# Performance work log

Hardware: AMD Instinct MI355X
Metric: run time of the kernel (lower is better)

The kernel has to match this reference:

```python
import jax, jax.numpy as jnp
import numpy as np

DIM = 1024
HEADS = 16
DIM_HEAD = 64
INNER = HEADS * DIM_HEAD  # 1024
EPS = 1e-5


def setup_inputs() -> dict:
    key = jax.random.key(0)
    ks = jax.random.split(key, 5)
    x = jax.random.normal(ks[0], (4, 2048, DIM), dtype=jnp.float32)
    ln_gamma = jnp.ones((DIM,), dtype=jnp.float32)
    ln_beta = jnp.zeros((DIM,), dtype=jnp.float32)
    # nn.Linear weights ~ U(-1/sqrt(fan_in), 1/sqrt(fan_in)); stored as (out, in) in torch,
    # here kept as (in, out) for x @ W.
    lim = 1.0 / np.sqrt(DIM)
    w_qkv = jax.random.uniform(ks[1], (DIM, 3 * INNER), minval=-lim, maxval=lim, dtype=jnp.float32)
    lim2 = 1.0 / np.sqrt(INNER)
    w_out = jax.random.uniform(ks[2], (INNER, DIM), minval=-lim2, maxval=lim2, dtype=jnp.float32)
    return {"x": x, "ln_gamma": ln_gamma, "ln_beta": ln_beta, "w_qkv": w_qkv, "w_out": w_out}


def reference(x, ln_gamma, ln_beta, w_qkv, w_out):
    b, n, d = x.shape
    # LayerNorm
    mu = jnp.mean(x, axis=-1, keepdims=True)
    var = jnp.mean(jnp.square(x - mu), axis=-1, keepdims=True)
    xn = (x - mu) * jax.lax.rsqrt(var + EPS) * ln_gamma + ln_beta
    # QKV projection
    qkv = xn @ w_qkv  # (b, n, 3*inner)
    q, k, v = jnp.split(qkv, 3, axis=-1)
    def to_heads(t):
        return t.reshape(b, n, HEADS, DIM_HEAD).transpose(0, 2, 1, 3)  # (b,h,n,dh)
    q, k, v = to_heads(q), to_heads(k), to_heads(v)
    scale = DIM_HEAD ** -0.5
    scores = jnp.einsum('bhqd,bhkd->bhqk', q, k) * scale
    causal = jnp.tril(jnp.ones((n, n), dtype=bool))
    scores = jnp.where(causal, scores, -jnp.inf)
    probs = jax.nn.softmax(scores, axis=-1)
    out = jnp.einsum('bhqk,bhkd->bhqd', probs, v)
    out = out.transpose(0, 2, 1, 3).reshape(b, n, INNER)
    return out @ w_out
```

## Files before the change

### kernel.cpp

```cpp
#include <hip/hip_runtime.h>
#include <hip/hip_bf16.h>

#define DIM 1024
#define HEADS 16
#define DH 64
#define SEQ 2048
#define BATCH 4
#define ROWS (BATCH * SEQ)
#define NQKV (3 * DIM)

typedef __attribute__((ext_vector_type(8))) __bf16 bf16x8;
typedef __attribute__((ext_vector_type(4))) __bf16 bf16x4;
typedef __attribute__((ext_vector_type(4))) float f32x4;

__device__ inline void gload16(const void* g, void* l) {
  __builtin_amdgcn_global_load_lds(
      (const __attribute__((address_space(1))) void*)g,
      (__attribute__((address_space(3))) void*)l, 16, 0, 0);
}

__device__ inline float fast_exp2(float x) {
#if __has_builtin(__builtin_amdgcn_exp2f)
  return __builtin_amdgcn_exp2f(x);
#else
  return exp2f(x);
#endif
}

__global__ __launch_bounds__(256) void ln_tc(
    const float* __restrict__ x, const float* __restrict__ gamma,
    const float* __restrict__ beta, __bf16* __restrict__ xnb,
    const float* __restrict__ wq, const float* __restrict__ wo,
    __bf16* __restrict__ qT, __bf16* __restrict__ oT) {
  __shared__ float red1[4], red2[4];
  __shared__ float tile[32][33];
  const int bid = blockIdx.x;
  const int tid = threadIdx.x;
  if (bid < ROWS) {
    const float4* xr = (const float4*)(x + (size_t)bid * DIM);
    float4 v = xr[tid];
    float s1 = v.x + v.y + v.z + v.w;
    float s2 = v.x * v.x + v.y * v.y + v.z * v.z + v.w * v.w;
#pragma unroll
    for (int d = 32; d > 0; d >>= 1) {
      s1 += __shfl_xor(s1, d);
      s2 += __shfl_xor(s2, d);
    }
    const int wave = tid >> 6, lane = tid & 63;
    if (lane == 0) { red1[wave] = s1; red2[wave] = s2; }
    __syncthreads();
    s1 = red1[0] + red1[1] + red1[2] + red1[3];
    s2 = red2[0] + red2[1] + red2[2] + red2[3];
    const float mean = s1 * (1.0f / DIM);
    const float var = s2 * (1.0f / DIM) - mean * mean;
    const float rstd = rsqrtf(var + 1e-5f);
    float4 g = ((const float4*)gamma)[tid];
    float4 b = ((const float4*)beta)[tid];
    bf16x4 o;
    o[0] = (__bf16)((v.x - mean) * rstd * g.x + b.x);
    o[1] = (__bf16)((v.y - mean) * rstd * g.y + b.y);
    o[2] = (__bf16)((v.z - mean) * rstd * g.z + b.z);
    o[3] = (__bf16)((v.w - mean) * rstd * g.w + b.w);
    *(bf16x4*)(xnb + (size_t)bid * DIM + tid * 4) = o;
  } else {
    const int id2 = bid - ROWS;
    int bx = id2 & 127;
    const int by = id2 >> 7;
    const int tx = tid & 31, ty = tid >> 5;
    const float* in;
    __bf16* out;
    int cols;
    if (bx < 96) {
      in = wq; out = qT; cols = NQKV;
    } else {
      in = wo; out = oT; cols = DIM; bx -= 96;
    }
    const int c0 = bx * 32, r0 = by * 32;
#pragma unroll
    for (int rr = ty; rr < 32; rr += 8)
      tile[rr][tx] = in[(size_t)(r0 + rr) * cols + c0 + tx];
    __syncthreads();
#pragma unroll
    for (int rr = ty; rr < 32; rr += 8)
      out[(size_t)(c0 + rr) * DIM + r0 + tx] = (__bf16)tile[tx][rr];
  }
}

template <int MODE>
__global__ __launch_bounds__(512, 1) void gemmP(
    const __bf16* __restrict__ A, const __bf16* __restrict__ Bt, const int K,
    const int N, float* __restrict__ Cout, __bf16* __restrict__ qb,
    __bf16* __restrict__ kb, __bf16* __restrict__ vtb) {
  __shared__ __bf16 As[3][2][128 * 64];
  __shared__ __bf16 Bs[3][128 * 64];
  const int tid = threadIdx.x;
  const int wave = tid >> 6, lane = tid & 63;
  const int quad = lane >> 4, l16 = lane & 15;
  const int wm = wave >> 2, wn = wave & 3;

  const int i = (int)blockIdx.x;
  const int xcd = i & 7;
  const int j = i >> 3;
  const int ntn = N >> 7;
  const int mgrp = j / ntn;
  const int ntl = j - mgrp * ntn;
  const size_t tileM = (size_t)(xcd + (mgrp << 3)) * 256;
  const size_t tileN = (size_t)ntl * 128;
  const int sel = (MODE == 1) ? (int)(tileN >> 10) : 0;
  const bool vmode = (MODE == 1) && (sel == 2);

  f32x4 acc[8][2];
#pragma unroll
  for (int a = 0; a < 8; ++a)
#pragma unroll
    for (int b = 0; b < 2; ++b) acc[a][b] = (f32x4){0.f, 0.f, 0.f, 0.f};

  const __bf16* Abase = A + tileM * (size_t)K;
  const __bf16* Bbase = Bt + tileN * (size_t)K;

  const int slr = tid >> 3, sc = tid & 7;
  const int scol = (sc ^ (slr & 7)) << 3;

  auto stageA = [&](int buf, int h, int kt) {
    const size_t col = (size_t)(kt << 6) + scol;
#pragma unroll
    for (int p = 0; p < 2; ++p) {
      const int gr = p * 128 + h * 64 + slr;
      const int lr = p * 64 + slr;
      gload16(Abase + (size_t)gr * K + col, &As[buf][h][lr * 64 + sc * 8]);
    }
  };
  auto stageB = [&](int buf, int kt) {
    const size_t col = (size_t)(kt << 6) + scol;
#pragma unroll
    for (int p = 0; p < 2; ++p) {
      const int lr = p * 64 + slr;
      gload16(Bbase + (size_t)lr * K + col, &Bs[buf][lr * 64 + sc * 8]);
    }
  };
  auto stageTile = [&](int buf, int kt) {
    stageA(buf, 0, kt);
    stageB(buf, kt);
    stageA(buf, 1, kt);
  };

  const int rpc = quad ^ (l16 & 7);
  auto ldA = [&](int buf, int mt, int ks) -> bf16x8 {
    const int lr = wm * 64 + (mt & 3) * 16 + l16;
    return *(const bf16x8*)&As[buf][mt >> 2][lr * 64 + ((rpc ^ (ks << 2)) << 3)];
  };
  auto ldB = [&](int buf, int nt, int ks) -> bf16x8 {
    const int lr = wn * 32 + nt * 16 + l16;
    return *(const bf16x8*)&Bs[buf][lr * 64 + ((rpc ^ (ks << 2)) << 3)];
  };

  auto cluster = [&](const bf16x8* af, bf16x8 bf0, bf16x8 bf1, int mb) {
    __builtin_amdgcn_s_setprio(1);
    if (vmode) {
#pragma unroll
      for (int mt = 0; mt < 4; ++mt) {
        acc[mb + mt][0] = __builtin_amdgcn_mfma_f32_16x16x32_bf16(
            af[mt], bf0, acc[mb + mt][0], 0, 0, 0);
        acc[mb + mt][1] = __builtin_amdgcn_mfma_f32_16x16x32_bf16(
            af[mt], bf1, acc[mb + mt][1], 0, 0, 0);
      }
    } else {
#pragma unroll
      for (int mt = 0; mt < 4; ++mt) {
        acc[mb + mt][0] = __builtin_amdgcn_mfma_f32_16x16x32_bf16(
            bf0, af[mt], acc[mb + mt][0], 0, 0, 0);
        acc[mb + mt][1] = __builtin_amdgcn_mfma_f32_16x16x32_bf16(
            bf1, af[mt], acc[mb + mt][1], 0, 0, 0);
      }
    }
    __builtin_amdgcn_s_setprio(0);
  };

  stageTile(0, 0);
  stageTile(1, 1);

  const int NT = K >> 6;
  int bufc = 0;
  bf16x8 af[4], b00, b01, b10, b11;

  for (int t = 0; t < NT; ++t) {
    if (t < NT - 1)
      asm volatile("s_waitcnt vmcnt(6)" ::: "memory");
    else
      asm volatile("s_waitcnt vmcnt(0)" ::: "memory");
    __builtin_amdgcn_s_barrier();
    asm volatile("" ::: "memory");
    __builtin_amdgcn_sched_barrier(0);

    if (t + 2 < NT) {
      const int sb = bufc + 2 >= 3 ? bufc - 1 : bufc + 2;
      stageTile(sb, t + 2);
    }

#pragma unroll
    for (int mt = 0; mt < 4; ++mt) af[mt] = ldA(bufc, mt, 0);
    b00 = ldB(bufc, 0, 0);
    b01 = ldB(bufc, 1, 0);
    cluster(af, b00, b01, 0);
#pragma unroll
    for (int mt = 0; mt < 4; ++mt) af[mt] = ldA(bufc, mt, 1);
    b10 = ldB(bufc, 0, 1);
    b11 = ldB(bufc, 1, 1);
    cluster(af, b10, b11, 0);
#pragma unroll
    for (int mt = 0; mt < 4; ++mt) af[mt] = ldA(bufc, 4 + mt, 0);
    cluster(af, b00, b01, 4);
#pragma unroll
    for (int mt = 0; mt < 4; ++mt) af[mt] = ldA(bufc, 4 + mt, 1);
    cluster(af, b10, b11, 4);

    bufc = bufc == 2 ? 0 : bufc + 1;
  }

  if (MODE == 0) {
#pragma unroll
    for (int mt = 0; mt < 8; ++mt) {
      const size_t m = tileM + wm * 128 + mt * 16 + l16;
#pragma unroll
      for (int nt = 0; nt < 2; ++nt) {
        const size_t n0 = tileN + wn * 32 + nt * 16 + quad * 4;
        *(f32x4*)&Cout[m * (size_t)N + n0] = acc[mt][nt];
      }
    }
  } else if (sel < 2) {
    __bf16* dst = (sel == 0) ? qb : kb;
#pragma unroll
    for (int mt = 0; mt < 8; ++mt) {
      const size_t m = tileM + wm * 128 + mt * 16 + l16;
      const int b = (int)(m >> 11), seq = (int)(m & 2047);
#pragma unroll
      for (int nt = 0; nt < 2; ++nt) {
        const int c = (int)(tileN & 1023) + wn * 32 + nt * 16 + quad * 4;
        const int head = c >> 6, dh = c & 63;
        bf16x4 pk;
#pragma unroll
        for (int r = 0; r < 4; ++r) pk[r] = (__bf16)acc[mt][nt][r];
        *(bf16x4*)&dst[(((size_t)b * HEADS + head) * SEQ + seq) * DH + dh] = pk;
      }
    }
  } else {
#pragma unroll
    for (int nt = 0; nt < 2; ++nt) {
      const int c = (int)(tileN & 1023) + wn * 32 + nt * 16 + l16;
      const int head = c >> 6, dh = c & 63;
#pragma unroll
      for (int mt = 0; mt < 8; ++mt) {
        const size_t m0 = tileM + wm * 128 + mt * 16 + quad * 4;
        const int b = (int)(m0 >> 11), seq = (int)(m0 & 2047);
        bf16x4 pk;
#pragma unroll
        for (int r = 0; r < 4; ++r) pk[r] = (__bf16)acc[mt][nt][r];
        *(bf16x4*)&vtb[(((size_t)b * HEADS + head) * DH + dh) * SEQ + seq] = pk;
      }
    }
  }
}

__global__ __launch_bounds__(256, 4) void attn_kernel(
    const __bf16* __restrict__ qb, const __bf16* __restrict__ kb,
    const __bf16* __restrict__ vtb, __bf16* __restrict__ ob) {
  const int bh = blockIdx.x;
  const int by = blockIdx.y;
  const int tid = threadIdx.x;
  const int wave = tid >> 6, lane = tid & 63;
  const int quad = lane >> 4, l16 = lane & 15;

  __shared__ __bf16 Ks[2][64 * 64];
  __shared__ __bf16 Vs[2][64 * 64];
  __shared__ __bf16 Ps[4][16 * 36];

  const __bf16* kg = kb + (size_t)bh * SEQ * DH;
  const __bf16* vg = vtb + (size_t)bh * DH * SEQ;

  const int i1 = by, i2 = 31 - by;
  const int T = 33;

  const int kr = lane >> 3, kc = lane & 7;

  auto stage = [&](int buf, int j) {
#pragma unroll
    for (int p = 0; p < 2; ++p) {
      const int rbase = wave * 16 + p * 8;
      const int row = rbase + kr;
      gload16(kg + (size_t)(j * 64 + row) * DH + ((kc ^ (row & 7)) << 3),
              &Ks[buf][rbase * 64]);
      gload16(vg + (size_t)row * SEQ + j * 64 + ((kc ^ (row & 7)) << 3),
              &Vs[buf][rbase * 64]);
    }
  };

  const float QSCALE = 0.125f * 1.44269504088896f;
  bf16x8 qf[2];
  auto load_q = [&](int i) {
    const __bf16* qbase = qb + ((size_t)bh * SEQ + (size_t)i * 64 + wave * 16) * DH;
#pragma unroll
    for (int ks = 0; ks < 2; ++ks) {
      bf16x8 v = *(const bf16x8*)(qbase + l16 * DH + ks * 32 + quad * 8);
#pragma unroll
      for (int e = 0; e < 8; ++e) v[e] = (__bf16)((float)v[e] * QSCALE);
      qf[ks] = v;
    }
  };

  float m_i, l_i;
  f32x4 o_acc[4];
  auto reset_state = [&]() {
    m_i = -1e30f;
    l_i = 0.f;
#pragma unroll
    for (int md = 0; md < 4; ++md) o_acc[md] = (f32x4){0.f, 0.f, 0.f, 0.f};
  };
  const int b_out = bh >> 4, h_out = bh & 15;
  auto epilogue = [&](int i) {
    float lsum = l_i;
    lsum += __shfl_xor(lsum, 16);
    lsum += __shfl_xor(lsum, 32);
    const float inv = __builtin_amdgcn_rcpf(lsum);
    const int seq = i * 64 + wave * 16 + l16;
    __bf16* dst = ob + ((size_t)b_out * SEQ + seq) * DIM + h_out * DH;
#pragma unroll
    for (int md = 0; md < 4; ++md) {
      bf16x4 pk;
#pragma unroll
      for (int r = 0; r < 4; ++r) pk[r] = (__bf16)(o_acc[md][r] * inv);
      *(bf16x4*)(dst + md * 16 + quad * 4) = pk;
    }
  };

  load_q(i1);
  reset_state();
  stage(0, 0);

  for (int t = 0; t < T; ++t) {
    __syncthreads();
    if (t + 1 < T) {
      const int jn = (t + 1 <= by) ? (t + 1) : (t - by);
      stage((t + 1) & 1, jn);
    }
    const int buf = t & 1;
    const int i = (t <= by) ? i1 : i2;
    const int j = (t <= by) ? t : (t - by - 1);
    const bool diag = (j == i);

    f32x4 sa[4];
#pragma unroll
    for (int nt = 0; nt < 4; ++nt) sa[nt] = (f32x4){0.f, 0.f, 0.f, 0.f};
    __builtin_amdgcn_s_setprio(1);
#pragma unroll
    for (int nt = 0; nt < 4; ++nt)
#pragma unroll
      for (int ks = 0; ks < 2; ++ks) {
        bf16x8 kf = *(const bf16x8*)&Ks[buf][(nt * 16 + l16) * 64 +
                                            (((ks * 4 + quad) ^ (l16 & 7)) << 3)];
        sa[nt] = __builtin_amdgcn_mfma_f32_16x16x32_bf16(kf, qf[ks], sa[nt], 0, 0, 0);
      }
    __builtin_amdgcn_s_setprio(0);

    if (diag) {
      const int qrl = wave * 16 + l16;
#pragma unroll
      for (int nt = 0; nt < 4; ++nt)
#pragma unroll
        for (int r = 0; r < 4; ++r) {
          const int kvl = nt * 16 + quad * 4 + r;
          if (kvl > qrl) sa[nt][r] = -1e30f;
        }
    }

    {
      float mx = -1e30f;
#pragma unroll
      for (int nt = 0; nt < 4; ++nt) {
        const float a0 = fmaxf(fmaxf(sa[nt][0], sa[nt][1]), sa[nt][2]);
        mx = fmaxf(mx, fmaxf(a0, sa[nt][3]));
      }
      mx = fmaxf(mx, __shfl_xor(mx, 16));
      mx = fmaxf(mx, __shfl_xor(mx, 32));
      if (__all(mx - m_i <= 8.f)) {
        float rs = 0.f;
#pragma unroll
        for (int nt = 0; nt < 4; ++nt)
#pragma unroll
          for (int r = 0; r < 4; ++r) {
            const float p = fast_exp2(sa[nt][r] - m_i);
            sa[nt][r] = p;
            rs += p;
          }
        l_i += rs;
      } else {
        const float mnew = fmaxf(m_i, mx);
        const float alpha = fast_exp2(m_i - mnew);
        m_i = mnew;
        float rs = 0.f;
#pragma unroll
        for (int nt = 0; nt < 4; ++nt)
#pragma unroll
          for (int r = 0; r < 4; ++r) {
            const float p = fast_exp2(sa[nt][r] - mnew);
            sa[nt][r] = p;
            rs += p;
          }
        l_i = l_i * alpha + rs;
#pragma unroll
        for (int md = 0; md < 4; ++md)
#pragma unroll
          for (int r = 0; r < 4; ++r) o_acc[md][r] *= alpha;
      }
    }

#pragma unroll
    for (int c = 0; c < 2; ++c) {
#pragma unroll
      for (int ntl = 0; ntl < 2; ++ntl) {
        const int nt = c * 2 + ntl;
        bf16x4 pk;
#pragma unroll
        for (int r = 0; r < 4; ++r) pk[r] = (__bf16)sa[nt][r];
        *(bf16x4*)&Ps[wave][l16 * 36 + ntl * 16 + quad * 4] = pk;
      }
      bf16x8 pf = *(const bf16x8*)&Ps[wave][l16 * 36 + quad * 8];
      __builtin_amdgcn_s_setprio(1);
#pragma unroll
      for (int md = 0; md < 4; ++md) {
        bf16x8 vf = *(const bf16x8*)&Vs[buf][(md * 16 + l16) * 64 +
                                            (((c * 4 + quad) ^ (l16 & 7)) << 3)];
        o_acc[md] = __builtin_amdgcn_mfma_f32_16x16x32_bf16(vf, pf, o_acc[md], 0, 0, 0);
      }
      __builtin_amdgcn_s_setprio(0);
    }

    if (t == by) {
      epilogue(i1);
      reset_state();
      load_q(i2);
    }
  }
  epilogue(i2);
}

extern "C" void kernel_launch(void* const* d_in, const int* in_sizes, int n_in,
                              void* d_out, int out_size, void* d_ws, size_t ws_size,
                              hipStream_t stream) {
  const float* x = (const float*)d_in[0];
  const float* gamma = (const float*)d_in[1];
  const float* beta = (const float*)d_in[2];
  const float* w_qkv = (const float*)d_in[3];
  const float* w_out = (const float*)d_in[4];
  float* out = (float*)d_out;

  char* ws = (char*)d_ws;
  const size_t MB = 1024 * 1024;
  __bf16* xnb = (__bf16*)ws;
  __bf16* wqkvT = (__bf16*)(ws + 16 * MB);
  __bf16* woutT = (__bf16*)(ws + 24 * MB);
  __bf16* qbuf = (__bf16*)(ws + 32 * MB);
  __bf16* kbuf = (__bf16*)(ws + 48 * MB);
  __bf16* vtbuf = (__bf16*)(ws + 64 * MB);
  __bf16* attnb = xnb;

  ln_tc<<<ROWS + 4096, 256, 0, stream>>>(x, gamma, beta, xnb, w_qkv, w_out,
                                         wqkvT, woutT);
  gemmP<1><<<dim3((ROWS / 256) * (NQKV / 128)), 512, 0, stream>>>(
      xnb, wqkvT, DIM, NQKV, nullptr, qbuf, kbuf, vtbuf);
  attn_kernel<<<dim3(BATCH * HEADS, 16), 256, 0, stream>>>(qbuf, kbuf, vtbuf, attnb);
  gemmP<0><<<dim3((ROWS / 256) * (DIM / 128)), 512, 0, stream>>>(
      attnb, woutT, DIM, DIM, out, nullptr, nullptr, nullptr);
}
```

Baseline: 272.7 us.

## Process 128-row query tiles per attention block and drop XCD-aware GEMM tile swizzle

The attention kernel now gives each wave two 16-row query groups, so each block covers 128 query rows. K fragments are loaded from LDS once and reused across both groups, halving K/V staging per query row and doubling MFMA work per LDS read. The grid halves to 8 blocks per head, paired so causal work stays balanced, and launch bounds drop to 2 blocks per CU to allow the extra registers. Separately, the GEMM launches switch from a 1D XCD-swizzled tile mapping to a plain 2D grid, which may change L2 locality across XCDs.

Result: slower. 278.8 us (+2.3%).

```diff
diff --git a/kernel.cpp b/kernel.cpp
--- a/kernel.cpp
+++ b/kernel.cpp
@@ -98,14 +98,8 @@
   const int quad = lane >> 4, l16 = lane & 15;
   const int wm = wave >> 2, wn = wave & 3;
 
-  const int i = (int)blockIdx.x;
-  const int xcd = i & 7;
-  const int j = i >> 3;
-  const int ntn = N >> 7;
-  const int mgrp = j / ntn;
-  const int ntl = j - mgrp * ntn;
-  const size_t tileM = (size_t)(xcd + (mgrp << 3)) * 256;
-  const size_t tileN = (size_t)ntl * 128;
+  const size_t tileM = (size_t)blockIdx.x * 256;
+  const size_t tileN = (size_t)blockIdx.y * 128;
   const int sel = (MODE == 1) ? (int)(tileN >> 10) : 0;
   const bool vmode = (MODE == 1) && (sel == 2);
 
@@ -261,7 +255,7 @@
   }
 }
 
-__global__ __launch_bounds__(256, 4) void attn_kernel(
+__global__ __launch_bounds__(256, 2) void attn_kernel(
     const __bf16* __restrict__ qb, const __bf16* __restrict__ kb,
     const __bf16* __restrict__ vtb, __bf16* __restrict__ ob) {
   const int bh = blockIdx.x;
@@ -272,13 +266,14 @@
 
   __shared__ __bf16 Ks[2][64 * 64];
   __shared__ __bf16 Vs[2][64 * 64];
-  __shared__ __bf16 Ps[4][16 * 36];
+  __shared__ __bf16 Ps[4][2][16 * 36];
 
   const __bf16* kg = kb + (size_t)bh * SEQ * DH;
   const __bf16* vg = vtb + (size_t)bh * DH * SEQ;
 
-  const int i1 = by, i2 = 31 - by;
-  const int T = 33;
+  const int i1 = by, i2 = 15 - by;
+  const int P0 = 2 * i1 + 2;
+  const int T = P0 + 2 * i2 + 2;
 
   const int kr = lane >> 3, kc = lane & 7;
 
@@ -295,40 +290,50 @@
   };
 
   const float QSCALE = 0.125f * 1.44269504088896f;
-  bf16x8 qf[2];
+  bf16x8 qf[2][2];
   auto load_q = [&](int i) {
-    const __bf16* qbase = qb + ((size_t)bh * SEQ + (size_t)i * 64 + wave * 16) * DH;
-#pragma unroll
-    for (int ks = 0; ks < 2; ++ks) {
-      bf16x8 v = *(const bf16x8*)(qbase + l16 * DH + ks * 32 + quad * 8);
-#pragma unroll
-      for (int e = 0; e < 8; ++e) v[e] = (__bf16)((float)v[e] * QSCALE);
-      qf[ks] = v;
-    }
-  };
-
-  float m_i, l_i;
-  f32x4 o_acc[4];
+#pragma unroll
+    for (int qg = 0; qg < 2; ++qg) {
+      const __bf16* qbase =
+          qb + ((size_t)bh * SEQ + (size_t)i * 128 + wave * 32 + qg * 16) * DH;
+#pragma unroll
+      for (int ks = 0; ks < 2; ++ks) {
+        bf16x8 v = *(const bf16x8*)(qbase + l16 * DH + ks * 32 + quad * 8);
+#pragma unroll
+        for (int e = 0; e < 8; ++e) v[e] = (__bf16)((float)v[e] * QSCALE);
+        qf[qg][ks] = v;
+      }
+    }
+  };
+
+  float m_i[2], l_i[2];
+  f32x4 o_acc[2][4];
   auto reset_state = [&]() {
-    m_i = -1e30f;
-    l_i = 0.f;
-#pragma unroll
-    for (int md = 0; md < 4; ++md) o_acc[md] = (f32x4){0.f, 0.f, 0.f, 0.f};
+#pragma unroll
+    for (int qg = 0; qg < 2; ++qg) {
+      m_i[qg] = -1e30f;
+      l_i[qg] = 0.f;
+#pragma unroll
+      for (int md = 0; md < 4; ++md) o_acc[qg][md] = (f32x4){0.f, 0.f, 0.f, 0.f};
+    }
   };
   const int b_out = bh >> 4, h_out = bh & 15;
   auto epilogue = [&](int i) {
-    float lsum = l_i;
-    lsum += __shfl_xor(lsum, 16);
-    lsum += __shfl_xor(lsum, 32);
-    const float inv = __builtin_amdgcn_rcpf(lsum);
-    const int seq = i * 64 + wave * 16 + l16;
-    __bf16* dst = ob + ((size_t)b_out * SEQ + seq) * DIM + h_out * DH;
-#pragma unroll
-    for (int md = 0; md < 4; ++md) {
-      bf16x4 pk;
-#pragma unroll
-      for (int r = 0; r < 4; ++r) pk[r] = (__bf16)(o_acc[md][r] * inv);
-      *(bf16x4*)(dst + md * 16 + quad * 4) = pk;
+#pragma unroll
+    for (int qg = 0; qg < 2; ++qg) {
+      float lsum = l_i[qg];
+      lsum += __shfl_xor(lsum, 16);
+      lsum += __shfl_xor(lsum, 32);
+      const float inv = __builtin_amdgcn_rcpf(lsum);
+      const int seq = i * 128 + wave * 32 + qg * 16 + l16;
+      __bf16* dst = ob + ((size_t)b_out * SEQ + seq) * DIM + h_out * DH;
+#pragma unroll
+      for (int md = 0; md < 4; ++md) {
+        bf16x4 pk;
+#pragma unroll
+        for (int r = 0; r < 4; ++r) pk[r] = (__bf16)(o_acc[qg][md][r] * inv);
+        *(bf16x4*)(dst + md * 16 + quad * 4) = pk;
+      }
     }
   };
 
@@ -339,102 +344,119 @@
   for (int t = 0; t < T; ++t) {
     __syncthreads();
     if (t + 1 < T) {
-      const int jn = (t + 1 <= by) ? (t + 1) : (t - by);
+      const int jn = (t + 1 < P0) ? (t + 1) : (t + 1 - P0);
       stage((t + 1) & 1, jn);
     }
     const int buf = t & 1;
-    const int i = (t <= by) ? i1 : i2;
-    const int j = (t <= by) ? t : (t - by - 1);
-    const bool diag = (j == i);
-
-    f32x4 sa[4];
-#pragma unroll
-    for (int nt = 0; nt < 4; ++nt) sa[nt] = (f32x4){0.f, 0.f, 0.f, 0.f};
+    const bool ph0 = (t < P0);
+    const int i = ph0 ? i1 : i2;
+    const int j = ph0 ? t : t - P0;
+
+    bf16x8 kfr[4][2];
+#pragma unroll
+    for (int nt = 0; nt < 4; ++nt)
+#pragma unroll
+      for (int ks = 0; ks < 2; ++ks)
+        kfr[nt][ks] = *(const bf16x8*)&Ks[buf][(nt * 16 + l16) * 64 +
+                                              (((ks * 4 + quad) ^ (l16 & 7)) << 3)];
+
+    f32x4 sa2[2][4];
+#pragma unroll
+    for (int qg = 0; qg < 2; ++qg)
+#pragma unroll
+      for (int nt = 0; nt < 4; ++nt) sa2[qg][nt] = (f32x4){0.f, 0.f, 0.f, 0.f};
     __builtin_amdgcn_s_setprio(1);
 #pragma unroll
-    for (int nt = 0; nt < 4; ++nt)
-#pragma unroll
-      for (int ks = 0; ks < 2; ++ks) {
-        bf16x8 kf = *(const bf16x8*)&Ks[buf][(nt * 16 + l16) * 64 +
-                                            (((ks * 4 + quad) ^ (l16 & 7)) << 3)];
-        sa[nt] = __builtin_amdgcn_mfma_f32_16x16x32_bf16(kf, qf[ks], sa[nt], 0, 0, 0);
-      }
+    for (int qg = 0; qg < 2; ++qg)
+#pragma unroll
+      for (int nt = 0; nt < 4; ++nt)
+#pragma unroll
+        for (int ks = 0; ks < 2; ++ks)
+          sa2[qg][nt] = __builtin_amdgcn_mfma_f32_16x16x32_bf16(
+              kfr[nt][ks], qf[qg][ks], sa2[qg][nt], 0, 0, 0);
     __builtin_amdgcn_s_setprio(0);
 
-    if (diag) {
-      const int qrl = wave * 16 + l16;
-#pragma unroll
-      for (int nt = 0; nt < 4; ++nt)
-#pragma unroll
-        for (int r = 0; r < 4; ++r) {
-          const int kvl = nt * 16 + quad * 4 + r;
-          if (kvl > qrl) sa[nt][r] = -1e30f;
-        }
-    }
-
-    {
+#pragma unroll
+    for (int qg = 0; qg < 2; ++qg) {
+      const int qrow0 = i * 128 + wave * 32 + qg * 16;
+      if (j * 64 + 63 > qrow0) {
+        const int qr = qrow0 + l16;
+#pragma unroll
+        for (int nt = 0; nt < 4; ++nt)
+#pragma unroll
+          for (int r = 0; r < 4; ++r) {
+            const int kv = j * 64 + nt * 16 + quad * 4 + r;
+            if (kv > qr) sa2[qg][nt][r] = -1e30f;
+          }
+      }
       float mx = -1e30f;
 #pragma unroll
       for (int nt = 0; nt < 4; ++nt) {
-        const float a0 = fmaxf(fmaxf(sa[nt][0], sa[nt][1]), sa[nt][2]);
-        mx = fmaxf(mx, fmaxf(a0, sa[nt][3]));
+        const float a0 = fmaxf(fmaxf(sa2[qg][nt][0], sa2[qg][nt][1]), sa2[qg][nt][2]);
+        mx = fmaxf(mx, fmaxf(a0, sa2[qg][nt][3]));
       }
       mx = fmaxf(mx, __shfl_xor(mx, 16));
       mx = fmaxf(mx, __shfl_xor(mx, 32));
-      if (__all(mx - m_i <= 8.f)) {
+      if (__all(mx - m_i[qg] <= 8.f)) {
         float rs = 0.f;
 #pragma unroll
         for (int nt = 0; nt < 4; ++nt)
 #pragma unroll
           for (int r = 0; r < 4; ++r) {
-            const float p = fast_exp2(sa[nt][r] - m_i);
-            sa[nt][r] = p;
+            const float p = fast_exp2(sa2[qg][nt][r] - m_i[qg]);
+            sa2[qg][nt][r] = p;
             rs += p;
           }
-        l_i += rs;
+        l_i[qg] += rs;
       } else {
-        const float mnew = fmaxf(m_i, mx);
-        const float alpha = fast_exp2(m_i - mnew);
-        m_i = mnew;
+        const float mnew = fmaxf(m_i[qg], mx);
+        const float alpha = fast_exp2(m_i[qg] - mnew);
+        m_i[qg] = mnew;
         float rs = 0.f;
 #pragma unroll
         for (int nt = 0; nt < 4; ++nt)
 #pragma unroll
           for (int r = 0; r < 4; ++r) {
-            const float p = fast_exp2(sa[nt][r] - mnew);
-            sa[nt][r] = p;
+            const float p = fast_exp2(sa2[qg][nt][r] - mnew);
+            sa2[qg][nt][r] = p;
             rs += p;
           }
-        l_i = l_i * alpha + rs;
+        l_i[qg] = l_i[qg] * alpha + rs;
 #pragma unroll
         for (int md = 0; md < 4; ++md)
 #pragma unroll
-          for (int r = 0; r < 4; ++r) o_acc[md][r] *= alpha;
+          for (int r = 0; r < 4; ++r) o_acc[qg][md][r] *= alpha;
       }
     }
 
 #pragma unroll
     for (int c = 0; c < 2; ++c) {
 #pragma unroll
-      for (int ntl = 0; ntl < 2; ++ntl) {
-        const int nt = c * 2 + ntl;
-        bf16x4 pk;
-#pragma unroll
-        for (int r = 0; r < 4; ++r) pk[r] = (__bf16)sa[nt][r];
-        *(bf16x4*)&Ps[wave][l16 * 36 + ntl * 16 + quad * 4] = pk;
-      }
-      bf16x8 pf = *(const bf16x8*)&Ps[wave][l16 * 36 + quad * 8];
+      for (int qg = 0; qg < 2; ++qg)
+#pragma unroll
+        for (int ntl = 0; ntl < 2; ++ntl) {
+          const int nt = c * 2 + ntl;
+          bf16x4 pk;
+#pragma unroll
+          for (int r = 0; r < 4; ++r) pk[r] = (__bf16)sa2[qg][nt][r];
+          *(bf16x4*)&Ps[wave][qg][l16 * 36 + ntl * 16 + quad * 4] = pk;
+        }
+      bf16x8 pf0 = *(const bf16x8*)&Ps[wave][0][l16 * 36 + quad * 8];
+      bf16x8 pf1 = *(const bf16x8*)&Ps[wave][1][l16 * 36 + quad * 8];
       __builtin_amdgcn_s_setprio(1);
 #pragma unroll
       for (int md = 0; md < 4; ++md) {
         bf16x8 vf = *(const bf16x8*)&Vs[buf][(md * 16 + l16) * 64 +
                                             (((c * 4 + quad) ^ (l16 & 7)) << 3)];
-        o_acc[md] = __builtin_amdgcn_mfma_f32_16x16x32_bf16(vf, pf, o_acc[md], 0, 0, 0);
+        o_acc[0][md] =
+            __builtin_amdgcn_mfma_f32_16x16x32_bf16(vf, pf0, o_acc[0][md], 0, 0, 0);
+        o_acc[1][md] =
+            __builtin_amdgcn_mfma_f32_16x16x32_bf16(vf, pf1, o_acc[1][md], 0, 0, 0);
       }
       __builtin_amdgcn_s_setprio(0);
     }
 
-    if (t == by) {
+    if (t == P0 - 1) {
       epilogue(i1);
       reset_state();
       load_q(i2);
@@ -465,9 +487,9 @@
 
   ln_tc<<<ROWS + 4096, 256, 0, stream>>>(x, gamma, beta, xnb, w_qkv, w_out,
                                          wqkvT, woutT);
-  gemmP<1><<<dim3((ROWS / 256) * (NQKV / 128)), 512, 0, stream>>>(
+  gemmP<1><<<dim3(ROWS / 256, NQKV / 128), 512, 0, stream>>>(
       xnb, wqkvT, DIM, NQKV, nullptr, qbuf, kbuf, vtbuf);
-  attn_kernel<<<dim3(BATCH * HEADS, 16), 256, 0, stream>>>(qbuf, kbuf, vtbuf, attnb);
-  gemmP<0><<<dim3((ROWS / 256) * (DIM / 128)), 512, 0, stream>>>(
+  attn_kernel<<<dim3(BATCH * HEADS, 8), 256, 0, stream>>>(qbuf, kbuf, vtbuf, attnb);
+  gemmP<0><<<dim3(ROWS / 256, DIM / 128), 512, 0, stream>>>(
       attnb, woutT, DIM, DIM, out, nullptr, nullptr, nullptr);
 }
```
